# Kernel tuning notes

Hardware: AMD Instinct MI355X
Metric: run time of the kernel (lower is better)

## Reference

```python
import jax, jax.numpy as jnp
import numpy as np

GAMMA = 1.0
INF = 1e8  # large finite value standing in for +inf (keeps vjp NaN-free)


def _pairwise_sq_dist(x, y):
    # x: (B, N, d), y: (B, M, d) -> (B, N, M) squared Euclidean distances
    x2 = jnp.sum(x * x, axis=-1)
    y2 = jnp.sum(y * y, axis=-1)
    xy = jnp.einsum('bnd,bmd->bnm', x, y)
    return x2[:, :, None] + y2[:, None, :] - 2.0 * xy


def _soft_dtw(D, gamma=GAMMA):
    # Soft-DTW DP via anti-diagonal wavefront scan.
    # R[i,j] = D[i,j] + softmin(R[i-1,j-1], R[i-1,j], R[i,j-1])
    # softmin(a,b,c) = -gamma * logsumexp(-[a,b,c]/gamma)
    B, N, M = D.shape
    i_idx = jnp.arange(N)

    def step(carry, d):
        r2, r1 = carry  # diagonals d-2 and d-1, each (B, N) indexed by i
        j = d - i_idx  # column index for each row i on diagonal d
        valid = (j >= 0) & (j < M)
        first = (i_idx == 0)[None, :]
        # R[i-1, j-1] lives at index i-1 of diagonal d-2; R[-1,-1] = 0 for (0,0)
        a = jnp.where(first, jnp.where(d == 0, 0.0, INF), jnp.roll(r2, 1, axis=1))
        # R[i-1, j] lives at index i-1 of diagonal d-1
        b = jnp.where(first, INF, jnp.roll(r1, 1, axis=1))
        # R[i, j-1] lives at index i of diagonal d-1
        c = r1
        dv = jnp.take_along_axis(D, jnp.clip(j, 0, M - 1)[None, :, None], axis=2)[:, :, 0]
        sm = -gamma * jax.nn.logsumexp(jnp.stack([-a, -b, -c]) / gamma, axis=0)
        rnew = jnp.where(valid[None, :], dv + sm, INF)
        return (r1, rnew), None

    init = (jnp.full((B, N), INF, D.dtype), jnp.full((B, N), INF, D.dtype))
    (_, rlast), _ = jax.lax.scan(step, init, jnp.arange(N + M - 1))
    # last diagonal (d = N+M-2) holds R[N-1, M-1] at index i = N-1
    return rlast[:, N - 1]


def _sdtw_normalized(x, y):
    # normalize=True: sdtw(x,y) - 0.5*(sdtw(x,x) + sdtw(y,y)); batch all three DPs
    xs = jnp.concatenate([x, x, y], axis=0)
    ys = jnp.concatenate([y, x, y], axis=0)
    r = _soft_dtw(_pairwise_sq_dist(xs, ys))
    B = x.shape[0]
    return r[:B] - 0.5 * (r[B:2 * B] + r[2 * B:])


def setup_inputs() -> dict:
    key = jax.random.key(0)
    k1, k2 = jax.random.split(key)
    outputs = jax.random.normal(k1, (128, 256, 64), dtype=jnp.float32)
    targets = jax.random.normal(k2, (128, 256, 64), dtype=jnp.float32)
    return {"outputs": outputs, "targets": targets}


def reference(outputs, targets):
    # dis_func == 'Soft_DTW' branch: mean(soft-DTW) + 1e-5
    return _sdtw_normalized(outputs, targets).mean() + 1e-5
```

## Files before the change

### kernel.cpp

```cpp
#include <hip/hip_runtime.h>
#include <hip/hip_bf16.h>

#define NSEQ 256
#define DIM 64
#define NB 128
#define NPAIR 384
#define FINF 1e8f
#define LOG2E 1.4426950408889634f
#define LN2 0.6931471805599453f

using f32x4 = __attribute__((ext_vector_type(4))) float;
using s16x8 = __attribute__((ext_vector_type(8))) short;

__device__ __forceinline__ unsigned short bf16u(float f) {
    __hip_bfloat16 h = __float2bfloat16(f);
    return __builtin_bit_cast(unsigned short, h);
}
__device__ __forceinline__ short bf16s(float f) {
    __hip_bfloat16 h = __float2bfloat16(f);
    return __builtin_bit_cast(short, h);
}
__device__ __forceinline__ float min3f(float a, float b, float c) {
    float d; asm("v_min3_f32 %0, %1, %2, %3" : "=v"(d) : "v"(a), "v"(b), "v"(c));
    return d;
}
__device__ __forceinline__ float max3f(float a, float b, float c) {
    float d; asm("v_max3_f32 %0, %1, %2, %3" : "=v"(d) : "v"(a), "v"(b), "v"(c));
    return d;
}

__global__ __launch_bounds__(256, 3)
void dist_kernel(const float* __restrict__ X, const float* __restrict__ Y,
                 unsigned short* __restrict__ S) {
    __shared__ __align__(16) short b_lds[NSEQ * DIM];
    __shared__ __align__(16) short a_lds[128 * DIM];
    __shared__ float a2[128];
    __shared__ float b2[NSEQ];
    unsigned short* sbuf = reinterpret_cast<unsigned short*>(b_lds);

    const int bid = blockIdx.x;
    const int p = bid >> 1;
    const int h = bid & 1;
    const int b = p & (NB - 1);
    const int g = p >> 7;
    const float* Arow = (g == 2 ? Y : X) + (size_t)b * NSEQ * DIM
                        + (size_t)h * 128 * DIM;
    const float* Brow = (g == 1 ? X : Y) + (size_t)b * NSEQ * DIM;

    const int t = threadIdx.x;
    {
        const float4* bv = reinterpret_cast<const float4*>(Brow) + t * (DIM / 4);
        float sb = 0.f;
#pragma unroll
        for (int q = 0; q < 8; ++q) {
            float4 b0 = bv[2 * q], b1 = bv[2 * q + 1];
            sb += b0.x * b0.x + b0.y * b0.y + b0.z * b0.z + b0.w * b0.w
                + b1.x * b1.x + b1.y * b1.y + b1.z * b1.z + b1.w * b1.w;
            s16x8 pb = { bf16s(b0.x), bf16s(b0.y), bf16s(b0.z), bf16s(b0.w),
                         bf16s(b1.x), bf16s(b1.y), bf16s(b1.z), bf16s(b1.w) };
            *reinterpret_cast<s16x8*>(&b_lds[t * DIM + ((q ^ (t & 7)) << 3)]) = pb;
        }
        b2[t] = sb;
    }
    if (t < 128) {
        const float4* av = reinterpret_cast<const float4*>(Arow) + t * (DIM / 4);
        float sa = 0.f;
#pragma unroll
        for (int q = 0; q < 8; ++q) {
            float4 a0 = av[2 * q], a1 = av[2 * q + 1];
            sa += a0.x * a0.x + a0.y * a0.y + a0.z * a0.z + a0.w * a0.w
                + a1.x * a1.x + a1.y * a1.y + a1.z * a1.z + a1.w * a1.w;
            s16x8 pa = { bf16s(a0.x), bf16s(a0.y), bf16s(a0.z), bf16s(a0.w),
                         bf16s(a1.x), bf16s(a1.y), bf16s(a1.z), bf16s(a1.w) };
            *reinterpret_cast<s16x8*>(&a_lds[t * DIM + ((q ^ (t & 7)) << 3)]) = pa;
        }
        a2[t] = sa;
    }
    __syncthreads();

    const int wave = t >> 6;
    const int lane = t & 63;
    const int lrow = lane & 15;
    const int lk   = lane >> 4;

    s16x8 bfr[4][2];
    float bn[4];
#pragma unroll
    for (int ct = 0; ct < 4; ++ct) {
        const int c = 64 * wave + ct * 16 + lrow;
#pragma unroll
        for (int kk = 0; kk < 2; ++kk) {
            const int kb = kk * 4 + lk;
            bfr[ct][kk] = *reinterpret_cast<const s16x8*>(
                &b_lds[c * DIM + ((kb ^ (c & 7)) << 3)]);
        }
        bn[ct] = b2[c];
    }
    __syncthreads();

    const size_t pbase = (size_t)p * (NSEQ * NSEQ);
#pragma unroll 1
    for (int sloc = 0; sloc < 2; ++sloc) {
        const int rl0 = sloc * 64;
        const int r0  = h * 128 + rl0;
        s16x8 afr[4][2];
#pragma unroll
        for (int rt = 0; rt < 4; ++rt) {
            const int rl = rl0 + rt * 16 + lrow;
#pragma unroll
            for (int kk = 0; kk < 2; ++kk) {
                const int kb = kk * 4 + lk;
                afr[rt][kk] = *reinterpret_cast<const s16x8*>(
                    &a_lds[rl * DIM + ((kb ^ (rl & 7)) << 3)]);
            }
        }
#pragma unroll
        for (int ct = 0; ct < 4; ++ct) {
            const int c = 64 * wave + ct * 16 + lrow;
#pragma unroll
            for (int rt = 0; rt < 4; ++rt) {
                f32x4 acc = {0.f, 0.f, 0.f, 0.f};
                acc = __builtin_amdgcn_mfma_f32_16x16x32_bf16(afr[rt][0], bfr[ct][0], acc, 0, 0, 0);
                acc = __builtin_amdgcn_mfma_f32_16x16x32_bf16(afr[rt][1], bfr[ct][1], acc, 0, 0, 0);
#pragma unroll
                for (int jv = 0; jv < 4; ++jv) {
                    const int rloc = rt * 16 + lk * 4 + jv;
                    const float dist = a2[rl0 + rloc] + bn[ct] - 2.f * acc[jv];
                    sbuf[rloc * NSEQ + (c ^ (((rloc >> 2) & 3) << 4))] = bf16u(dist);
                }
            }
        }
        __syncthreads();
        const int sl = lane >> 4;
        const int q  = lane & 15;
#pragma unroll
        for (int gg = 0; gg < 16; ++gg) {
            const int s = 64 * wave + gg * 4 + sl;
            const int il0 = 4 * q;
            const int swz = ((q & 3) << 4);
            const int j0 = (s - (r0 + il0 + 0)) & 255;
            const int j1 = (s - (r0 + il0 + 1)) & 255;
            const int j2 = (s - (r0 + il0 + 2)) & 255;
            const int j3 = (s - (r0 + il0 + 3)) & 255;
            unsigned int e0 = sbuf[(il0 + 0) * NSEQ + (j0 ^ swz)];
            unsigned int e1 = sbuf[(il0 + 1) * NSEQ + (j1 ^ swz)];
            unsigned int e2 = sbuf[(il0 + 2) * NSEQ + (j2 ^ swz)];
            unsigned int e3 = sbuf[(il0 + 3) * NSEQ + (j3 ^ swz)];
            uint2 w;
            w.x = e0 | (e1 << 16);
            w.y = e2 | (e3 << 16);
            *reinterpret_cast<uint2*>(&S[pbase + (size_t)s * NSEQ + r0 + 4 * q]) = w;
        }
        __syncthreads();
    }
}

__global__ __launch_bounds__(256, 1)
void dtw_kernel(const unsigned short* __restrict__ S, float* __restrict__ rout) {
    __shared__ __align__(16) unsigned short sdD[4 * 4 * 1024];
    __shared__ __align__(16) float bndN[4][4][18];
    const int p = blockIdx.x;
    const int t = threadIdx.x;
    const int w = t >> 6;
    const int L = t & 63;
    const unsigned short* Sp = S + (size_t)p * (NSEQ * NSEQ);
    const int cfirst = 4 * w, clast = 4 * w + 19;
    const int lrow = L >> 3, lcol = L & 7;
    const bool lz = (L == 0);

    auto stageck = [&](int cc) {
        const int slot = cc & 3;
#pragma unroll
        for (int k = 0; k < 2; ++k) {
            const int row = (16 * cc + 8 * k + lrow) & 255;
            const char* src = (const char*)Sp + row * 512 + w * 128 + lcol * 16;
            __builtin_amdgcn_global_load_lds(
                (const __attribute__((address_space(1))) void*)src,
                (__attribute__((address_space(3))) void*)
                    &sdD[w * 4096 + slot * 1024 + k * 512],
                16, 0, 0);
        }
    };

    stageck(cfirst); stageck(cfirst + 1); stageck(cfirst + 2);

    float s1 = FINF, s2 = FINF, rp = FINF;
    const int finf_bits = __builtin_bit_cast(int, FINF);
    float out_val = 0.f;

    auto stepfn = [&](float dv2, float bt, float btm1) -> float {
        const float bb = lz ? bt : s1;
        const float a  = lz ? btm1 : s2;
        const float m   = min3f(a, bb, rp);
        const float med = __builtin_amdgcn_fmed3f(a, bb, rp);
        const float M   = max3f(a, bb, rp);
        const float x1 = fmaxf(m - med, -126.0f);
        const float x2 = fmaxf(m - M,   -126.0f);
        const float e1 = __builtin_bit_cast(float,
            (int)__builtin_fmaf(x1, 8388608.0f, 1064992212.0f));
        const float e2 = __builtin_bit_cast(float,
            (int)__builtin_fmaf(x2, 8388608.0f, 1064992212.0f));
        const float e = 1.0f + (e1 + e2);
        const float lg = __builtin_fmaf((float)__builtin_bit_cast(int, e),
                                        1.1920929e-7f, -126.94269504f);
        const float rn = (m - lg) + dv2;
        s2 = s1;
        s1 = __builtin_bit_cast(float,
            __builtin_amdgcn_update_dpp(finf_bits, __builtin_bit_cast(int, rn),
                                        0x138 , 0xF, 0xF, false));
        rp = rn;
        return rn;
    };

#pragma unroll 1
    for (int r = 0; r < 35; ++r) {
        __syncthreads();
        const int c = r - w;
        if (c >= cfirst && c <= clast) {
            if (c + 3 <= clast) stageck(c + 3);
            float dvv[16];
            {
                const unsigned short* db = &sdD[w * 4096 + (c & 3) * 1024 + L];
#pragma unroll
                for (int u = 0; u < 16; ++u)
                    dvv[u] = __builtin_bit_cast(float,
                                 (unsigned)db[u * 64] << 16) * LOG2E;
            }
            float bwf[16], carA, carB;
            if (w == 0) {
#pragma unroll
                for (int u = 0; u < 16; ++u) bwf[u] = FINF;
                carA = FINF;
                carB = (c == 0) ? 0.f : FINF;
            } else {
                const float* bs = &bndN[w][c & 3][0];
                carB = bs[0];
                carA = bs[1];
#pragma unroll
                for (int u = 0; u < 16; ++u) bwf[u] = bs[2 + u];
            }
            float rb[16];
            rb[0] = stepfn(dvv[0], carA, carB);
            rb[1] = stepfn(dvv[1], bwf[0], carA);
#pragma unroll
            for (int u = 2; u < 16; ++u)
                rb[u] = stepfn(dvv[u], bwf[u - 1], bwf[u - 2]);

            if (w < 3) {
                if (L == 63) {
                    float* bd = &bndN[w + 1][c & 3][0];
#pragma unroll
                    for (int u = 0; u < 16; ++u) bd[2 + u] = rb[u];
                    float* bd2 = &bndN[w + 1][(c + 1) & 3][0];
                    bd2[0] = rb[14];
                    bd2[1] = rb[15];
                }
            } else if (c == 31 && L == 63) {
                out_val = rb[14];
            }
        }
    }

    if (w == 3 && L == 63) rout[p] = out_val * LN2;
}

__global__ void reduce_kernel(const float* __restrict__ rr, float* __restrict__ out) {
    const int t = threadIdx.x;
    float v = rr[t] - 0.5f * (rr[t + 128] + rr[t + 256]);
#pragma unroll
    for (int o = 32; o > 0; o >>= 1) v += __shfl_down(v, o);
    __shared__ float sred[2];
    if ((t & 63) == 0) sred[t >> 6] = v;
    __syncthreads();
    if (t == 0) out[0] = (sred[0] + sred[1]) * (1.f / 128.f) + 1e-5f;
}

extern "C" void kernel_launch(void* const* d_in, const int* in_sizes, int n_in,
                              void* d_out, int out_size, void* d_ws, size_t ws_size,
                              hipStream_t stream) {
    const float* X = (const float*)d_in[0];
    const float* Y = (const float*)d_in[1];
    float* out = (float*)d_out;

    const size_t dbytes = (size_t)NPAIR * NSEQ * NSEQ * sizeof(unsigned short);
    const size_t need = dbytes + (size_t)NPAIR * sizeof(float);
    if (ws_size < need) {
        hipMemsetAsync(d_out, 0x7f, sizeof(float), stream);
        return;
    }
    unsigned short* Sws = (unsigned short*)d_ws;
    float* rws = (float*)((char*)d_ws + dbytes);

    dist_kernel<<<2 * NPAIR, 256, 0, stream>>>(X, Y, Sws);
    dtw_kernel<<<NPAIR, 256, 0, stream>>>(Sws, rws);
    reduce_kernel<<<1, 128, 0, stream>>>(rws, out);
}
```

Baseline: 91.99 us.

## Replace per-round block barriers with wave-level flag sync and larger DTW chunks

The soft-DTW wavefront kernel stops using a block-wide __syncthreads each round. Waves now signal each other through shared-memory progress counters (producer progress and consumer read progress) and spin with s_sleep. Chunks grow from 16 to 32 anti-diagonal steps, so there are fewer rounds, and staging uses a 3-slot ring with explicit vmcnt waits. Launch bounds move to 2 blocks per CU to allow co-residency. The risks are spin-wait overhead, higher register pressure from the 32-element arrays, and subtle memory-ordering correctness in the hand-rolled flags.

```diff
diff --git a/kernel.cpp b/kernel.cpp
--- a/kernel.cpp
+++ b/kernel.cpp
@@ -155,34 +155,39 @@
     }
 }
 
-__global__ __launch_bounds__(256, 1)
+__global__ __launch_bounds__(256, 2)
 void dtw_kernel(const unsigned short* __restrict__ S, float* __restrict__ rout) {
-    __shared__ __align__(16) unsigned short sdD[4 * 4 * 1024];
-    __shared__ __align__(16) float bndN[4][4][18];
-    const int p = blockIdx.x;
+    __shared__ __align__(16) unsigned short sdD[4 * 3 * 2048];
+    __shared__ __align__(16) float bndN[4][3][34];
+    __shared__ volatile int prog[4];
+    __shared__ volatile int rdprog[4];
     const int t = threadIdx.x;
     const int w = t >> 6;
     const int L = t & 63;
+    const int p = blockIdx.x;
     const unsigned short* Sp = S + (size_t)p * (NSEQ * NSEQ);
-    const int cfirst = 4 * w, clast = 4 * w + 19;
+    const int cfirst = 2 * w, clast = 2 * w + 9;
     const int lrow = L >> 3, lcol = L & 7;
     const bool lz = (L == 0);
 
+    if (L == 0) { prog[w] = -1000; rdprog[w] = cfirst - 1; }
+    __syncthreads();
+
     auto stageck = [&](int cc) {
-        const int slot = cc & 3;
-#pragma unroll
-        for (int k = 0; k < 2; ++k) {
-            const int row = (16 * cc + 8 * k + lrow) & 255;
+        const int slot = cc % 3;
+#pragma unroll
+        for (int k = 0; k < 4; ++k) {
+            const int row = (32 * cc + 8 * k + lrow) & 255;
             const char* src = (const char*)Sp + row * 512 + w * 128 + lcol * 16;
             __builtin_amdgcn_global_load_lds(
                 (const __attribute__((address_space(1))) void*)src,
                 (__attribute__((address_space(3))) void*)
-                    &sdD[w * 4096 + slot * 1024 + k * 512],
+                    &sdD[w * 6144 + slot * 2048 + k * 512],
                 16, 0, 0);
         }
     };
 
-    stageck(cfirst); stageck(cfirst + 1); stageck(cfirst + 2);
+    stageck(cfirst); stageck(cfirst + 1);
 
     float s1 = FINF, s2 = FINF, rp = FINF;
     const int finf_bits = __builtin_bit_cast(int, FINF);
@@ -213,52 +218,63 @@
     };
 
 #pragma unroll 1
-    for (int r = 0; r < 35; ++r) {
-        __syncthreads();
-        const int c = r - w;
-        if (c >= cfirst && c <= clast) {
-            if (c + 3 <= clast) stageck(c + 3);
-            float dvv[16];
-            {
-                const unsigned short* db = &sdD[w * 4096 + (c & 3) * 1024 + L];
-#pragma unroll
-                for (int u = 0; u < 16; ++u)
-                    dvv[u] = __builtin_bit_cast(float,
-                                 (unsigned)db[u * 64] << 16) * LOG2E;
+    for (int c = cfirst; c <= clast; ++c) {
+        if (w < 3) {
+            while (rdprog[w + 1] < c - 2) __builtin_amdgcn_s_sleep(2);
+        }
+        if (w > 0 && c <= 2 * w + 7) {
+            while (prog[w - 1] < c) __builtin_amdgcn_s_sleep(2);
+        }
+        asm volatile("" ::: "memory");
+        if (c < clast) asm volatile("s_waitcnt vmcnt(4)" ::: "memory");
+        else           asm volatile("s_waitcnt vmcnt(0)" ::: "memory");
+
+        float dvv[32];
+        {
+            const unsigned short* db = &sdD[w * 6144 + (c % 3) * 2048 + L];
+#pragma unroll
+            for (int u = 0; u < 32; ++u)
+                dvv[u] = __builtin_bit_cast(float,
+                             (unsigned)db[u * 64] << 16) * LOG2E;
+        }
+        float bwf[32], carA, carB;
+        if (w == 0) {
+#pragma unroll
+            for (int u = 0; u < 32; ++u) bwf[u] = FINF;
+            carA = FINF;
+            carB = (c == 0) ? 0.f : FINF;
+        } else {
+            const float* bs = &bndN[w][c % 3][0];
+            carB = bs[0];
+            carA = bs[1];
+#pragma unroll
+            for (int u = 0; u < 32; ++u) bwf[u] = bs[2 + u];
+        }
+        if (c + 2 <= clast) stageck(c + 2);
+
+        float rb[32];
+        rb[0] = stepfn(dvv[0], carA, carB);
+        rb[1] = stepfn(dvv[1], bwf[0], carA);
+#pragma unroll
+        for (int u = 2; u < 32; ++u)
+            rb[u] = stepfn(dvv[u], bwf[u - 1], bwf[u - 2]);
+
+        if (w < 3) {
+            if (L == 63) {
+                float* bd = &bndN[w + 1][c % 3][0];
+#pragma unroll
+                for (int u = 0; u < 32; ++u) bd[2 + u] = rb[u];
+                float* bd2 = &bndN[w + 1][(c + 1) % 3][0];
+                bd2[0] = rb[30];
+                bd2[1] = rb[31];
             }
-            float bwf[16], carA, carB;
-            if (w == 0) {
-#pragma unroll
-                for (int u = 0; u < 16; ++u) bwf[u] = FINF;
-                carA = FINF;
-                carB = (c == 0) ? 0.f : FINF;
-            } else {
-                const float* bs = &bndN[w][c & 3][0];
-                carB = bs[0];
-                carA = bs[1];
-#pragma unroll
-                for (int u = 0; u < 16; ++u) bwf[u] = bs[2 + u];
-            }
-            float rb[16];
-            rb[0] = stepfn(dvv[0], carA, carB);
-            rb[1] = stepfn(dvv[1], bwf[0], carA);
-#pragma unroll
-            for (int u = 2; u < 16; ++u)
-                rb[u] = stepfn(dvv[u], bwf[u - 1], bwf[u - 2]);
-
-            if (w < 3) {
-                if (L == 63) {
-                    float* bd = &bndN[w + 1][c & 3][0];
-#pragma unroll
-                    for (int u = 0; u < 16; ++u) bd[2 + u] = rb[u];
-                    float* bd2 = &bndN[w + 1][(c + 1) & 3][0];
-                    bd2[0] = rb[14];
-                    bd2[1] = rb[15];
-                }
-            } else if (c == 31 && L == 63) {
-                out_val = rb[14];
-            }
-        }
+            asm volatile("s_waitcnt lgkmcnt(0)" ::: "memory");
+            if (L == 63) prog[w] = c;
+        } else if (c == 15 && L == 63) {
+            out_val = rb[30];
+        }
+        asm volatile("" ::: "memory");
+        if (w > 0 && L == 0) rdprog[w] = c;
     }
 
     if (w == 3 && L == 63) rout[p] = out_val * LN2;
```

Result: faster. 88.99 us (-3.3%).
